# Performance work log

Measured on AMD Instinct MI355X. Metric: run time of the kernel, lower is better.

## Reference

```python
import jax, jax.numpy as jnp
import numpy as np

P = 16          # patch size
IMG = 224       # image size
EPS_COMBINE = 2.220446049250313e-16  # np.finfo(float).eps
NOISE_EPS = 0.01
LOSS_COEF = 1e-2
K = 1


def _patchify(x):
    # x: [B, C, H, W] -> [B, n_patches, C*P*P] (channel-major flatten, matching conv weight layout)
    B, C, H, W = x.shape
    gh, gw = H // P, W // P
    x = x.reshape(B, C, gh, P, gw, P)
    x = x.transpose(0, 2, 4, 1, 3, 5).reshape(B, gh * gw, C * P * P)
    return x


def _cv_squared(v):
    # squared coefficient of variation; torch .var() is unbiased (ddof=1)
    return jnp.var(v, ddof=1) / (jnp.mean(v) ** 2 + 1e-10)


def _norm_cdf(v):
    return jax.scipy.stats.norm.cdf(v)


def setup_inputs() -> dict:
    key = jax.random.key(0)
    ks = jax.random.split(key, 7)
    B, E, D_IN = 64, 8, 320
    x = jax.random.normal(ks[0], (B, 3, IMG, IMG), dtype=jnp.float32)
    g = jax.random.normal(ks[1], (B, D_IN), dtype=jnp.float32)
    noise = jax.random.normal(ks[2], (B, E), dtype=jnp.float32)
    w_gate = jax.random.normal(ks[3], (D_IN, E), dtype=jnp.float32) * 0.02
    w_noise = jax.random.normal(ks[4], (D_IN, E), dtype=jnp.float32) * 0.02
    w_exp = jax.random.normal(ks[5], (E, 768, 3, P, P), dtype=jnp.float32) * 0.02
    b_exp = jnp.zeros((E, 768), dtype=jnp.float32)
    return {"x": x, "g": g, "noise": noise, "w_gate": w_gate,
            "w_noise": w_noise, "w_exp": w_exp, "b_exp": b_exp}


def reference(x, g, noise, w_gate, w_noise, w_exp, b_exp):
    B = x.shape[0]
    E = w_gate.shape[1]

    # ---- noisy top-k gating (train mode) ----
    clean_logits = g @ w_gate                                   # [B, E]
    noise_stddev = jax.nn.softplus(g @ w_noise) + NOISE_EPS     # [B, E]
    noisy_logits = clean_logits + noise * noise_stddev          # [B, E]

    top_logits, top_idx = jax.lax.top_k(noisy_logits, K + 1)    # [B, K+1]
    top_k_gates = jax.nn.softmax(top_logits[:, :K], axis=1)     # [B, K]
    gates = jnp.zeros_like(noisy_logits).at[
        jnp.arange(B)[:, None], top_idx[:, :K]].set(top_k_gates)  # [B, E]

    # load: prob each expert's noisy logit lands in top-k (differentiable balance term)
    thr_in = top_logits[:, K][:, None]       # (k+1)-th value per row
    thr_out = top_logits[:, K - 1][:, None]  # k-th value per row
    is_in = noisy_logits > thr_in
    prob = jnp.where(is_in,
                     _norm_cdf((clean_logits - thr_in) / noise_stddev),
                     _norm_cdf((clean_logits - thr_out) / noise_stddev))
    load = prob.sum(0)                                           # [E]
    importance = gates.sum(0)                                    # [E]
    loss = (_cv_squared(importance) + _cv_squared(load)) * LOSS_COEF

    # ---- experts: per-expert patch-embed conv == patchify + GEMM ----
    patches = _patchify(x)                                       # [B, 196, 768]
    wf = w_exp.reshape(E, w_exp.shape[1], -1)                    # [E, out=768, in=768]
    y_exp = jnp.einsum('bpi,eoi->ebpo', patches, wf) + b_exp[:, None, None, :]  # [E,B,196,768]

    # ---- gate-weighted combine (dense equivalent of dispatch/combine) ----
    y = jnp.einsum('be,ebpo->bpo', gates, y_exp)                 # [B, 196, 768]
    y = jnp.where(y == 0, jnp.asarray(EPS_COMBINE, y.dtype), y)  # combined[combined==0] = eps
    return y, loss
```

## Files before the change

### kernel.cpp

```cpp
#include <hip/hip_runtime.h>
#include <math.h>

typedef unsigned short u16;
typedef unsigned int   u32;

using bf16x8 = __attribute__((ext_vector_type(8))) short;
using f32x4  = __attribute__((ext_vector_type(4))) float;

#define NB   64
#define NE   8
#define DIN  320
#define NP   196
#define CK   768
#define CN   768
#define ESTR (768 * 768)
#define NKT  24

#define GATE_BLOCKS  8
#define WCONV_BLOCKS 1152
#define PATCH_BLOCKS 2352

__device__ __forceinline__ u16 f2bf(float f) {
    u32 u = __builtin_bit_cast(u32, f);
    u += 0x7fffu + ((u >> 16) & 1u);
    return (u16)(u >> 16);
}

__device__ __forceinline__ void gload16(const void* g, void* l) {
    __builtin_amdgcn_global_load_lds(
        (const __attribute__((address_space(1))) void*)g,
        (__attribute__((address_space(3))) void*)l, 16, 0, 0);
}

__global__ __launch_bounds__(256) void prep1_kernel(
    const float* __restrict__ x,
    const float* __restrict__ g,
    const float* __restrict__ noise,
    const float* __restrict__ w_gate,
    const float* __restrict__ w_noise,
    const float* __restrict__ w_exp,
    float* __restrict__ gCl, float* __restrict__ gSd, float* __restrict__ gNy,
    u16* __restrict__ patches,
    u16* __restrict__ wb)
{
    __shared__ float sW[DIN][NE + 1];
    __shared__ float sWn[DIN][NE + 1];
    const int t = threadIdx.x;
    int bid = blockIdx.x;

    if (bid < GATE_BLOCKS) {
        for (int i = t; i < DIN * NE; i += 256) {
            sW[i >> 3][i & 7]  = w_gate[i];
            sWn[i >> 3][i & 7] = w_noise[i];
        }
        __syncthreads();
        const int pair = t >> 2, q = t & 3;
        const int bl = pair >> 3, e = pair & 7;
        const int b = bid * 8 + bl;
        float cl = 0.f, nz = 0.f;
        const float* gr = g + b * DIN + q * 80;
        #pragma unroll 4
        for (int j = 0; j < 80; ++j) {
            float gv = gr[j];
            cl = fmaf(gv, sW[q * 80 + j][e], cl);
            nz = fmaf(gv, sWn[q * 80 + j][e], nz);
        }
        cl += __shfl_xor(cl, 1); cl += __shfl_xor(cl, 2);
        nz += __shfl_xor(nz, 1); nz += __shfl_xor(nz, 2);
        if (q == 0) {
            int p = b * NE + e;
            float sd = fmaxf(nz, 0.f) + log1pf(expf(-fabsf(nz))) + 0.01f;
            gCl[p] = cl; gSd[p] = sd;
            gNy[p] = fmaf(noise[p], sd, cl);
        }
        return;
    }
    bid -= GATE_BLOCKS;

    if (bid < WCONV_BLOCKS) {
        int idx = bid * 256 + t;
        const float* src = w_exp + (size_t)idx * 16;
        u16* dst = wb + (size_t)idx * 16;
        float4 f0 = *reinterpret_cast<const float4*>(src);
        float4 f1 = *reinterpret_cast<const float4*>(src + 4);
        float4 f2 = *reinterpret_cast<const float4*>(src + 8);
        float4 f3 = *reinterpret_cast<const float4*>(src + 12);
        uint4 o0, o1;
        o0.x = (u32)f2bf(f0.x) | ((u32)f2bf(f0.y) << 16);
        o0.y = (u32)f2bf(f0.z) | ((u32)f2bf(f0.w) << 16);
        o0.z = (u32)f2bf(f1.x) | ((u32)f2bf(f1.y) << 16);
        o0.w = (u32)f2bf(f1.z) | ((u32)f2bf(f1.w) << 16);
        o1.x = (u32)f2bf(f2.x) | ((u32)f2bf(f2.y) << 16);
        o1.y = (u32)f2bf(f2.z) | ((u32)f2bf(f2.w) << 16);
        o1.z = (u32)f2bf(f3.x) | ((u32)f2bf(f3.y) << 16);
        o1.w = (u32)f2bf(f3.z) | ((u32)f2bf(f3.w) << 16);
        *reinterpret_cast<uint4*>(dst)     = o0;
        *reinterpret_cast<uint4*>(dst + 8) = o1;
        return;
    }
    bid -= WCONV_BLOCKS;

    int idx = bid * 256 + t;
    int ph = idx & 15;
    int c  = (idx >> 4) % 3;
    int p  = (idx / 48) % NP;
    int b  = idx / (48 * NP);
    const float* src = x + (((size_t)(b * 3 + c) * 224 + (p / 14) * 16 + ph) * 224
                            + (p % 14) * 16);
    u16* dst = patches + ((size_t)b * 256 + p) * CK + c * 256 + ph * 16;
    float4 f0 = *reinterpret_cast<const float4*>(src);
    float4 f1 = *reinterpret_cast<const float4*>(src + 4);
    float4 f2 = *reinterpret_cast<const float4*>(src + 8);
    float4 f3 = *reinterpret_cast<const float4*>(src + 12);
    uint4 o0, o1;
    o0.x = (u32)f2bf(f0.x) | ((u32)f2bf(f0.y) << 16);
    o0.y = (u32)f2bf(f0.z) | ((u32)f2bf(f0.w) << 16);
    o0.z = (u32)f2bf(f1.x) | ((u32)f2bf(f1.y) << 16);
    o0.w = (u32)f2bf(f1.z) | ((u32)f2bf(f1.w) << 16);
    o1.x = (u32)f2bf(f2.x) | ((u32)f2bf(f2.y) << 16);
    o1.y = (u32)f2bf(f2.z) | ((u32)f2bf(f2.w) << 16);
    o1.z = (u32)f2bf(f3.x) | ((u32)f2bf(f3.y) << 16);
    o1.w = (u32)f2bf(f3.z) | ((u32)f2bf(f3.w) << 16);
    *reinterpret_cast<uint4*>(dst)     = o0;
    *reinterpret_cast<uint4*>(dst + 8) = o1;
}

__global__ __launch_bounds__(512) void gate2_kernel(
    const float* __restrict__ gCl,
    const float* __restrict__ gSd,
    const float* __restrict__ gNy,
    int* __restrict__ eid,
    int* __restrict__ perm,
    float* __restrict__ loss_out)
{
    __shared__ float sNy[NB][NE];
    __shared__ float sProb[NB][NE];
    __shared__ int   sTop[NB];
    __shared__ float sImp[NE], sLoad[NE];
    const int t = threadIdx.x;
    const int b = t >> 3, e = t & 7;
    float cl = gCl[t], sd = gSd[t], ny = gNy[t];
    sNy[b][e] = ny;
    __syncthreads();
    float v1 = -1e30f, v2 = -1e30f; int i1 = 0;
    #pragma unroll
    for (int k2 = 0; k2 < NE; ++k2) {
        float v = sNy[b][k2];
        if (v > v1) { v2 = v1; v1 = v; i1 = k2; }
        else if (v > v2) { v2 = v; }
    }
    if (e == 0) { sTop[b] = i1; eid[b] = i1; }
    float thr = (ny > v2) ? v2 : v1;
    float z = (cl - thr) / sd;
    sProb[b][e] = 0.5f * (1.0f + erff(z * 0.7071067811865476f));
    __syncthreads();
    if (t < NE) {
        float imp = 0.f, ld = 0.f;
        for (int i = 0; i < NB; ++i) {
            imp += (sTop[i] == t) ? 1.0f : 0.0f;
            ld  += sProb[i][t];
        }
        sImp[t] = imp; sLoad[t] = ld;
    }
    __syncthreads();
    if (t == 0) {
        float mi = 0.f, ml = 0.f;
        for (int k2 = 0; k2 < NE; ++k2) { mi += sImp[k2]; ml += sLoad[k2]; }
        mi *= (1.0f / NE); ml *= (1.0f / NE);
        float vi = 0.f, vl = 0.f;
        for (int k2 = 0; k2 < NE; ++k2) {
            float d1 = sImp[k2] - mi;  vi += d1 * d1;
            float d2 = sLoad[k2] - ml; vl += d2 * d2;
        }
        vi *= (1.0f / (NE - 1)); vl *= (1.0f / (NE - 1));
        loss_out[0] = (vi / (mi * mi + 1e-10f) + vl / (ml * ml + 1e-10f)) * 0.01f;
        int off[NE]; int s = 0;
        #pragma unroll
        for (int k2 = 0; k2 < NE; ++k2) { off[k2] = s; s += (int)sImp[k2]; }
        for (int i = 0; i < NB; ++i) perm[off[sTop[i]]++] = i;
    }
}

__global__ __launch_bounds__(256, 5) void gemm_kernel(
    const u16* __restrict__ patches,
    const u16* __restrict__ wbf,
    const float* __restrict__ b_exp,
    const int* __restrict__ eid,
    const int* __restrict__ perm,
    float* __restrict__ out)
{
    __shared__ char smem[2][12288];

    const int id = blockIdx.x;
    const int v  = (id & 7) * 192 + (id >> 3);
    const int b  = perm[v / 24];
    const int rr = v % 24;
    const int mt = rr / 12;
    const int n0 = (rr % 12) * 64;
    const int e  = eid[b];

    const int t  = threadIdx.x;
    const int l  = t & 63;
    const int w  = t >> 6;

    const u32 cg = (u32)((l & 3) ^ (l >> 4));
    const u16* aS0 = patches + ((size_t)b * 256 + mt * 128 + (w << 4) + (l >> 2)) * CK + cg * 8;
    const u16* aS1 = aS0 + (size_t)64 * CK;
    const u16* bS  = wbf + (size_t)e * ESTR + ((size_t)n0 + (w << 4) + (l >> 2)) * CK + cg * 8;
    const u32 dA0 = ((u32)w << 10) + ((u32)l << 4);
    const u32 dA1 = dA0 + 4096;
    const u32 dB  = 8192u + dA0;

    u32 aOff[2], bOff[4];
    #pragma unroll
    for (int fm = 0; fm < 2; ++fm) {
        int row = w * 32 + fm * 16 + (l & 15);
        aOff[fm] = (u32)(row * 64) + (((u32)(l >> 4) ^ (u32)((row >> 2) & 3)) << 4);
    }
    #pragma unroll
    for (int fn = 0; fn < 4; ++fn) {
        int row = fn * 16 + (l & 15);
        bOff[fn] = 8192u + (u32)(row * 64) + (((u32)(l >> 4) ^ (u32)((row >> 2) & 3)) << 4);
    }

    f32x4 acc[2][4];
    #pragma unroll
    for (int fm = 0; fm < 2; ++fm)
        #pragma unroll
        for (int fn = 0; fn < 4; ++fn)
            acc[fm][fn] = (f32x4){0.f, 0.f, 0.f, 0.f};

    char* sm = &smem[0][0];

    gload16(aS0, sm + dA0);
    gload16(aS1, sm + dA1);
    gload16(bS,  sm + dB);

    for (int kt = 0; kt < NKT - 1; ++kt) {
        char* sn = sm + (u32)(((kt + 1) & 1) * 12288);
        gload16(aS0 + (kt + 1) * 32, sn + dA0);
        gload16(aS1 + (kt + 1) * 32, sn + dA1);
        gload16(bS  + (kt + 1) * 32, sn + dB);

        asm volatile("s_waitcnt vmcnt(3)" ::: "memory");
        __builtin_amdgcn_s_barrier();

        char* sc = sm + (u32)((kt & 1) * 12288);
        bf16x8 af[2], bfr[4];
        #pragma unroll
        for (int fm = 0; fm < 2; ++fm)
            af[fm] = *reinterpret_cast<const bf16x8*>(sc + aOff[fm]);
        #pragma unroll
        for (int fn = 0; fn < 4; ++fn)
            bfr[fn] = *reinterpret_cast<const bf16x8*>(sc + bOff[fn]);

        __builtin_amdgcn_s_setprio(1);
        #pragma unroll
        for (int fm = 0; fm < 2; ++fm)
            #pragma unroll
            for (int fn = 0; fn < 4; ++fn)
                acc[fm][fn] = __builtin_amdgcn_mfma_f32_16x16x32_bf16(
                    af[fm], bfr[fn], acc[fm][fn], 0, 0, 0);
        __builtin_amdgcn_s_setprio(0);

        __builtin_amdgcn_s_barrier();
    }

    asm volatile("s_waitcnt vmcnt(0)" ::: "memory");
    __builtin_amdgcn_s_barrier();
    {
        char* sc = sm + (u32)(((NKT - 1) & 1) * 12288);
        bf16x8 af[2], bfr[4];
        #pragma unroll
        for (int fm = 0; fm < 2; ++fm)
            af[fm] = *reinterpret_cast<const bf16x8*>(sc + aOff[fm]);
        #pragma unroll
        for (int fn = 0; fn < 4; ++fn)
            bfr[fn] = *reinterpret_cast<const bf16x8*>(sc + bOff[fn]);
        #pragma unroll
        for (int fm = 0; fm < 2; ++fm)
            #pragma unroll
            for (int fn = 0; fn < 4; ++fn)
                acc[fm][fn] = __builtin_amdgcn_mfma_f32_16x16x32_bf16(
                    af[fm], bfr[fn], acc[fm][fn], 0, 0, 0);
    }

    const int r4 = (l >> 4) * 4;
    #pragma unroll
    for (int fm = 0; fm < 2; ++fm) {
        int mb = mt * 128 + w * 32 + fm * 16 + r4;
        #pragma unroll
        for (int fn = 0; fn < 4; ++fn) {
            int col = n0 + fn * 16 + (l & 15);
            float bias = b_exp[e * CN + col];
            #pragma unroll
            for (int q = 0; q < 4; ++q) {
                int mrow = mb + q;
                if (mrow < NP) {
                    float vv = acc[fm][fn][q] + bias;
                    if (vv == 0.0f) vv = 2.220446049250313e-16f;
                    out[((size_t)b * NP + mrow) * CN + col] = vv;
                }
            }
        }
    }
}

extern "C" void kernel_launch(void* const* d_in, const int* in_sizes, int n_in,
                              void* d_out, int out_size, void* d_ws, size_t ws_size,
                              hipStream_t stream) {
    const float* x       = (const float*)d_in[0];
    const float* g       = (const float*)d_in[1];
    const float* noise   = (const float*)d_in[2];
    const float* w_gate  = (const float*)d_in[3];
    const float* w_noise = (const float*)d_in[4];
    const float* w_exp   = (const float*)d_in[5];
    const float* b_exp   = (const float*)d_in[6];
    float* out = (float*)d_out;

    char* ws = (char*)d_ws;
    int*   eid     = (int*)ws;
    int*   perm    = (int*)(ws + 256);
    float* gCl     = (float*)(ws + 512);
    float* gSd     = (float*)(ws + 2560);
    float* gNy     = (float*)(ws + 4608);
    u16*   patches = (u16*)(ws + 8192);
    u16*   wbf     = (u16*)(ws + 8192 + (size_t)NB * 256 * CK * 2);

    hipLaunchKernelGGL(prep1_kernel,
                       dim3(GATE_BLOCKS + WCONV_BLOCKS + PATCH_BLOCKS), dim3(256), 0, stream,
                       x, g, noise, w_gate, w_noise, w_exp, gCl, gSd, gNy, patches, wbf);
    hipLaunchKernelGGL(gate2_kernel, dim3(1), dim3(512), 0, stream,
                       gCl, gSd, gNy, eid, perm, out + (size_t)NB * NP * CN);
    hipLaunchKernelGGL(gemm_kernel, dim3(1536), dim3(256), 0, stream,
                       patches, wbf, b_exp, eid, perm, out);
}
```

Baseline: 69.32 us.

## Enlarge GEMM tiles to 128x192 with BK=64 and dynamic shared memory

The expert GEMM is retiled from 128x64 output tiles with a K-step of 32 to 128x192 tiles with a K-step of 64. Each of the four waves now computes a 64x96 sub-tile, and 80KB of dynamic LDS is double-buffered with an 8-way XOR swizzle. The grid shrinks from 1536 to 512 blocks and launch bounds drop to 2 blocks per CU. The aim is more MFMA work per LDS load and fewer barriers, in exchange for higher register pressure and lower occupancy. With only 512 blocks the tail and load balance across CUs may also get worse.

```diff
diff --git a/kernel.cpp b/kernel.cpp
--- a/kernel.cpp
+++ b/kernel.cpp
@@ -14,7 +14,7 @@
 #define CK   768
 #define CN   768
 #define ESTR (768 * 768)
-#define NKT  24
+#define NKT2 12
 
 #define GATE_BLOCKS  8
 #define WCONV_BLOCKS 1152
@@ -181,7 +181,7 @@
     }
 }
 
-__global__ __launch_bounds__(256, 5) void gemm_kernel(
+__global__ void __launch_bounds__(256, 2) gemm_kernel(
     const u16* __restrict__ patches,
     const u16* __restrict__ wbf,
     const float* __restrict__ b_exp,
@@ -189,109 +189,109 @@
     const int* __restrict__ perm,
     float* __restrict__ out)
 {
-    __shared__ char smem[2][12288];
+    extern __shared__ char sm[];
 
     const int id = blockIdx.x;
-    const int v  = (id & 7) * 192 + (id >> 3);
-    const int b  = perm[v / 24];
-    const int rr = v % 24;
-    const int mt = rr / 12;
-    const int n0 = (rr % 12) * 64;
+    const int v  = (id & 7) * 64 + (id >> 3);
+    const int b  = perm[v >> 3];
+    const int rr = v & 7;
+    const int m0 = (rr >> 2) * 128;
+    const int n0 = (rr & 3) * 192;
     const int e  = eid[b];
 
     const int t  = threadIdx.x;
     const int l  = t & 63;
     const int w  = t >> 6;
-
-    const u32 cg = (u32)((l & 3) ^ (l >> 4));
-    const u16* aS0 = patches + ((size_t)b * 256 + mt * 128 + (w << 4) + (l >> 2)) * CK + cg * 8;
-    const u16* aS1 = aS0 + (size_t)64 * CK;
-    const u16* bS  = wbf + (size_t)e * ESTR + ((size_t)n0 + (w << 4) + (l >> 2)) * CK + cg * 8;
-    const u32 dA0 = ((u32)w << 10) + ((u32)l << 4);
-    const u32 dA1 = dA0 + 4096;
-    const u32 dB  = 8192u + dA0;
-
-    u32 aOff[2], bOff[4];
-    #pragma unroll
-    for (int fm = 0; fm < 2; ++fm) {
-        int row = w * 32 + fm * 16 + (l & 15);
-        aOff[fm] = (u32)(row * 64) + (((u32)(l >> 4) ^ (u32)((row >> 2) & 3)) << 4);
-    }
-    #pragma unroll
-    for (int fn = 0; fn < 4; ++fn) {
-        int row = fn * 16 + (l & 15);
-        bOff[fn] = 8192u + (u32)(row * 64) + (((u32)(l >> 4) ^ (u32)((row >> 2) & 3)) << 4);
-    }
-
-    f32x4 acc[2][4];
-    #pragma unroll
-    for (int fm = 0; fm < 2; ++fm)
-        #pragma unroll
-        for (int fn = 0; fn < 4; ++fn)
+    const int wm = w >> 1;
+    const int wn = w & 1;
+
+    const u32 cg = (u32)((l & 7) ^ (l >> 3));
+    const u16* aS[4];
+    const u16* bS[6];
+    u32 aD[4], bD[6];
+    #pragma unroll
+    for (int j = 0; j < 4; ++j) {
+        int row = w * 32 + j * 8 + (l >> 3);
+        aS[j] = patches + ((size_t)b * 256 + m0 + row) * CK + cg * 8;
+        aD[j] = (u32)(w * 4096 + (j * 64 + l) * 16);
+    }
+    #pragma unroll
+    for (int j = 0; j < 6; ++j) {
+        int row = w * 48 + j * 8 + (l >> 3);
+        bS[j] = wbf + (size_t)e * ESTR + ((size_t)n0 + row) * CK + cg * 8;
+        bD[j] = 16384u + (u32)(w * 6144 + (j * 64 + l) * 16);
+    }
+
+    u32 aOff[2][4], bOff[2][6];
+    #pragma unroll
+    for (int ks = 0; ks < 2; ++ks) {
+        #pragma unroll
+        for (int fm = 0; fm < 4; ++fm) {
+            int row = wm * 64 + fm * 16 + (l & 15);
+            aOff[ks][fm] = (u32)(row * 128) + (((u32)(ks * 4 + (l >> 4)) ^ (u32)(l & 7)) << 4);
+        }
+        #pragma unroll
+        for (int fn = 0; fn < 6; ++fn) {
+            int row = wn * 96 + fn * 16 + (l & 15);
+            bOff[ks][fn] = 16384u + (u32)(row * 128)
+                         + (((u32)(ks * 4 + (l >> 4)) ^ (u32)(l & 7)) << 4);
+        }
+    }
+
+    f32x4 acc[4][6];
+    #pragma unroll
+    for (int fm = 0; fm < 4; ++fm)
+        #pragma unroll
+        for (int fn = 0; fn < 6; ++fn)
             acc[fm][fn] = (f32x4){0.f, 0.f, 0.f, 0.f};
 
-    char* sm = &smem[0][0];
-
-    gload16(aS0, sm + dA0);
-    gload16(aS1, sm + dA1);
-    gload16(bS,  sm + dB);
-
-    for (int kt = 0; kt < NKT - 1; ++kt) {
-        char* sn = sm + (u32)(((kt + 1) & 1) * 12288);
-        gload16(aS0 + (kt + 1) * 32, sn + dA0);
-        gload16(aS1 + (kt + 1) * 32, sn + dA1);
-        gload16(bS  + (kt + 1) * 32, sn + dB);
-
-        asm volatile("s_waitcnt vmcnt(3)" ::: "memory");
+    auto STAGE = [&](u32 bo, int kt) {
+        #pragma unroll
+        for (int j = 0; j < 4; ++j) gload16(aS[j] + kt * 64, sm + bo + aD[j]);
+        #pragma unroll
+        for (int j = 0; j < 6; ++j) gload16(bS[j] + kt * 64, sm + bo + bD[j]);
+    };
+    auto COMP = [&](u32 bo) {
+        #pragma unroll
+        for (int ks = 0; ks < 2; ++ks) {
+            bf16x8 af[4], bfr[6];
+            #pragma unroll
+            for (int fm = 0; fm < 4; ++fm)
+                af[fm] = *reinterpret_cast<const bf16x8*>(sm + bo + aOff[ks][fm]);
+            #pragma unroll
+            for (int fn = 0; fn < 6; ++fn)
+                bfr[fn] = *reinterpret_cast<const bf16x8*>(sm + bo + bOff[ks][fn]);
+            __builtin_amdgcn_s_setprio(1);
+            #pragma unroll
+            for (int fm = 0; fm < 4; ++fm)
+                #pragma unroll
+                for (int fn = 0; fn < 6; ++fn)
+                    acc[fm][fn] = __builtin_amdgcn_mfma_f32_16x16x32_bf16(
+                        af[fm], bfr[fn], acc[fm][fn], 0, 0, 0);
+            __builtin_amdgcn_s_setprio(0);
+        }
+    };
+
+    STAGE(0, 0);
+
+    for (int kt = 0; kt < NKT2 - 1; ++kt) {
+        STAGE((u32)(((kt + 1) & 1) * 40960), kt + 1);
+        asm volatile("s_waitcnt vmcnt(10)" ::: "memory");
         __builtin_amdgcn_s_barrier();
-
-        char* sc = sm + (u32)((kt & 1) * 12288);
-        bf16x8 af[2], bfr[4];
-        #pragma unroll
-        for (int fm = 0; fm < 2; ++fm)
-            af[fm] = *reinterpret_cast<const bf16x8*>(sc + aOff[fm]);
-        #pragma unroll
-        for (int fn = 0; fn < 4; ++fn)
-            bfr[fn] = *reinterpret_cast<const bf16x8*>(sc + bOff[fn]);
-
-        __builtin_amdgcn_s_setprio(1);
-        #pragma unroll
-        for (int fm = 0; fm < 2; ++fm)
-            #pragma unroll
-            for (int fn = 0; fn < 4; ++fn)
-                acc[fm][fn] = __builtin_amdgcn_mfma_f32_16x16x32_bf16(
-                    af[fm], bfr[fn], acc[fm][fn], 0, 0, 0);
-        __builtin_amdgcn_s_setprio(0);
-
+        COMP((u32)((kt & 1) * 40960));
         __builtin_amdgcn_s_barrier();
     }
-
     asm volatile("s_waitcnt vmcnt(0)" ::: "memory");
     __builtin_amdgcn_s_barrier();
-    {
-        char* sc = sm + (u32)(((NKT - 1) & 1) * 12288);
-        bf16x8 af[2], bfr[4];
-        #pragma unroll
-        for (int fm = 0; fm < 2; ++fm)
-            af[fm] = *reinterpret_cast<const bf16x8*>(sc + aOff[fm]);
-        #pragma unroll
-        for (int fn = 0; fn < 4; ++fn)
-            bfr[fn] = *reinterpret_cast<const bf16x8*>(sc + bOff[fn]);
-        #pragma unroll
-        for (int fm = 0; fm < 2; ++fm)
-            #pragma unroll
-            for (int fn = 0; fn < 4; ++fn)
-                acc[fm][fn] = __builtin_amdgcn_mfma_f32_16x16x32_bf16(
-                    af[fm], bfr[fn], acc[fm][fn], 0, 0, 0);
-    }
+    COMP((u32)(((NKT2 - 1) & 1) * 40960));
 
     const int r4 = (l >> 4) * 4;
     #pragma unroll
-    for (int fm = 0; fm < 2; ++fm) {
-        int mb = mt * 128 + w * 32 + fm * 16 + r4;
-        #pragma unroll
-        for (int fn = 0; fn < 4; ++fn) {
-            int col = n0 + fn * 16 + (l & 15);
+    for (int fm = 0; fm < 4; ++fm) {
+        int mb = m0 + wm * 64 + fm * 16 + r4;
+        #pragma unroll
+        for (int fn = 0; fn < 6; ++fn) {
+            int col = n0 + wn * 96 + fn * 16 + (l & 15);
             float bias = b_exp[e * CN + col];
             #pragma unroll
             for (int q = 0; q < 4; ++q) {
@@ -327,11 +327,14 @@
     u16*   patches = (u16*)(ws + 8192);
     u16*   wbf     = (u16*)(ws + 8192 + (size_t)NB * 256 * CK * 2);
 
+    hipFuncSetAttribute((const void*)gemm_kernel,
+                        hipFuncAttributeMaxDynamicSharedMemorySize, 81920);
+
     hipLaunchKernelGGL(prep1_kernel,
                        dim3(GATE_BLOCKS + WCONV_BLOCKS + PATCH_BLOCKS), dim3(256), 0, stream,
                        x, g, noise, w_gate, w_noise, w_exp, gCl, gSd, gNy, patches, wbf);
     hipLaunchKernelGGL(gate2_kernel, dim3(1), dim3(512), 0, stream,
                        gCl, gSd, gNy, eid, perm, out + (size_t)NB * NP * CN);
-    hipLaunchKernelGGL(gemm_kernel, dim3(1536), dim3(256), 0, stream,
+    hipLaunchKernelGGL(gemm_kernel, dim3(512), dim3(256), 81920, stream,
                        patches, wbf, b_exp, eid, perm, out);
 }
```

Result: faster. 64.05 us (-7.6%).
